# Optimization experiments

Measured on AMD Instinct MI355X. Metric: run time of the kernel, lower is better.

Reference implementation:

```python
import jax, jax.numpy as jnp
import numpy as np

IH = IW = 1024          # image size (iH, iW)
NMS_CAND = 1000         # dup_attrs['nms_candidates']
NMS_THR = 0.65          # dup_attrs['nms_thr']
MAX_SEGS = 100          # max_segs


def _mask_to_box(masks):
    # masks: [N, H, W] bool -> xyxy float boxes [N, 4] in pixel coords
    N, H, W = masks.shape
    rows = masks.any(axis=2)            # [N, H]
    cols = masks.any(axis=1)            # [N, W]
    x1 = jnp.argmax(cols, axis=1)
    x2 = W - jnp.argmax(cols[:, ::-1], axis=1)
    y1 = jnp.argmax(rows, axis=1)
    y2 = H - jnp.argmax(rows[:, ::-1], axis=1)
    return jnp.stack([x1, y1, x2, y2], axis=-1).astype(jnp.float32)


def _box_iou(b):
    # b: [K, 4] xyxy -> pairwise IoU [K, K]
    x1, y1, x2, y2 = b[:, 0], b[:, 1], b[:, 2], b[:, 3]
    area = (x2 - x1) * (y2 - y1)
    ix1 = jnp.maximum(x1[:, None], x1[None, :])
    iy1 = jnp.maximum(y1[:, None], y1[None, :])
    ix2 = jnp.minimum(x2[:, None], x2[None, :])
    iy2 = jnp.minimum(y2[:, None], y2[None, :])
    inter = jnp.clip(ix2 - ix1, 0.0) * jnp.clip(iy2 - iy1, 0.0)
    union = area[:, None] + area[None, :] - inter
    return inter / jnp.maximum(union, 1e-9)


def _greedy_nms_keep(iou, thr):
    # boxes assumed pre-sorted by descending score; returns keep mask [K]
    k = iou.shape[0]
    idx = jnp.arange(k)

    def body(i, keep):
        sup = keep[i] & (iou[i] > thr) & (idx > i)
        return keep & ~sup

    return jax.lax.fori_loop(0, k, body, jnp.ones((k,), dtype=bool))


def setup_inputs() -> dict:
    key = jax.random.key(0)
    k1, k2 = jax.random.split(key)
    cls_logits = jax.random.normal(k1, (300, 81), dtype=jnp.float32)
    seg_logits = jax.random.normal(k2, (300, 200, 200), dtype=jnp.float32)
    return {"cls_logits": cls_logits, "seg_logits": seg_logits}


def reference(cls_logits, seg_logits):
    N, fH, fW = seg_logits.shape
    C = cls_logits.shape[1] - 1  # last class is background/no-object

    # mask thresholding + emptiness flag (filtering replaced by score masking)
    pred_masks = seg_logits > 0                              # [N, fH, fW]
    non_empty = pred_masks.reshape(N, -1).sum(axis=1) > 0    # [N]

    # mask -> box for NMS
    boxes = _mask_to_box(pred_masks)                         # [N, 4]

    # sigmoid scoring over (feat, class); empty masks get score -1 (never picked)
    scores = jax.nn.sigmoid(cls_logits[:, :-1])              # [N, C]
    scores = jnp.where(non_empty[:, None], scores, -1.0).reshape(-1)  # [N*C]
    feat_ids = jnp.repeat(jnp.arange(N), C)                  # [N*C]
    labels = jnp.tile(jnp.arange(C), N)                      # [N*C]

    # top nms_candidates (scores sorted descending)
    k = min(NMS_CAND, N * C)
    cand_scores, cand_ids = jax.lax.top_k(scores, k)
    cand_feats = feat_ids[cand_ids]
    cand_labels = labels[cand_ids]
    cand_boxes = boxes[cand_feats]

    # batched (class-aware) NMS: offset boxes per label
    offset = cand_labels.astype(jnp.float32)[:, None] * (float(max(fH, fW)) + 1.0)
    iou = _box_iou(cand_boxes + offset)
    keep = _greedy_nms_keep(iou, NMS_THR) & (cand_scores >= 0.0)

    # keep top max_segs among survivors
    kept_scores = jnp.where(keep, cand_scores, -jnp.inf)
    sel_scores, sel = jax.lax.top_k(kept_scores, MAX_SEGS)
    sel_feats = cand_feats[sel]
    sel_labels = cand_labels[sel]

    # upsample selected mask logits to image size and threshold
    sel_logits = seg_logits[sel_feats]                       # [M, fH, fW]
    maps = jax.image.resize(sel_logits, (MAX_SEGS, IH, IW), method='bilinear')
    out_masks = maps > 0                                     # [M, iH, iW] bool
    batch_ids = jnp.zeros((MAX_SEGS,), dtype=jnp.int32)

    return sel_labels, out_masks, sel_scores, batch_ids
```

## Files before the change

kernel.cpp:

```cpp
#include <hip/hip_runtime.h>
#include <cstdint>
#include <cstddef>

typedef unsigned int u32;
typedef unsigned long long u64;
typedef float vf4 __attribute__((ext_vector_type(4)));

#define NF 300
#define NCLS 80
#define NCLS1 81
#define FH 200
#define FW 200
#define PIX 40000
#define NC 24000
#define KCAND 1000
#define CAP 4096
#define NBINS 65536
#define MAXSEG 100
#define OUT_MASK_OFF 100
#define OUT_SCORE_OFF 104857700
#define OUT_BATCH_OFF 104857800
#define NEG_BIG -3.3895313892515355e38f
#define RYC 8

#define WS_HIST      0u
#define WS_KEYS      262144u
#define WS_COLLECT   454144u
#define WS_CNT       486912u
#define WS_BOXES     486928u
#define WS_CLAB      496928u
#define WS_CFEAT     500928u
#define WS_CSCORE    504928u
#define WS_CBOX      508928u
#define WS_ROWBITS   524928u
#define WS_SELFEAT   656128u
#define WS_WTAB      656528u

__device__ __forceinline__ u32 ord32_r3(float f) {
  u32 b = __float_as_uint(f);
  return (b & 0x80000000u) ? ~b : (b | 0x80000000u);
}
__device__ __forceinline__ float unord32_r3(u32 o) {
  u32 b = (o & 0x80000000u) ? (o & 0x7FFFFFFFu) : ~o;
  return __uint_as_float(b);
}

__global__ void r3_init_wtab(u32* __restrict__ hist, u32* __restrict__ cnts,
                             float4* __restrict__ wtab) {
  int i = blockIdx.x * 256 + threadIdx.x;
  hist[i] = 0u;
  if (i < 4) cnts[i] = 0u;
  if (i < 1024) {
    float s = __fsub_rn(__fmul_rn((float)i + 0.5f, 0.1953125f), 0.5f);
    int j0 = (int)floorf(s);
    int j1 = j0 + 1;
    float w0 = fmaxf(0.f, __fsub_rn(1.f, fabsf(__fsub_rn(s, (float)j0))));
    float w1 = fmaxf(0.f, __fsub_rn(1.f, fabsf(__fsub_rn(s, (float)j1))));
    bool in0 = (j0 >= 0) && (j0 < FH);
    bool in1 = (j1 >= 0) && (j1 < FH);
    float tot = __fadd_rn(in0 ? w0 : 0.f, in1 ? w1 : 0.f);
    float w0n = in0 ? (w0 / tot) : 0.f;
    float w1n = in1 ? (w1 / tot) : 0.f;
    wtab[i] = make_float4(w0n, w1n, (float)max(j0, 0), (float)min(j1, FH - 1));
  }
}

__global__ void r3_boxes_scores(const float* __restrict__ seg, const float* __restrict__ cls,
                                float4* __restrict__ boxes, u64* __restrict__ keys,
                                u32* __restrict__ hist) {
  __shared__ int sminx[256], sminy[256], smaxx[256], smaxy[256];
  int n = blockIdx.x, t = threadIdx.x;
  const float4* img = (const float4*)(seg + (size_t)n * PIX);
  int minx = FW, miny = FH, maxx = -1, maxy = -1;
  for (int q = t; q < PIX / 4; q += 256) {
    float4 v = img[q];
    int p = q * 4;
    int y = p / FW;
    int x = p - y * FW;
    if (v.x > 0.f) { minx = min(minx, x);     maxx = max(maxx, x);     miny = min(miny, y); maxy = max(maxy, y); }
    if (v.y > 0.f) { minx = min(minx, x + 1); maxx = max(maxx, x + 1); miny = min(miny, y); maxy = max(maxy, y); }
    if (v.z > 0.f) { minx = min(minx, x + 2); maxx = max(maxx, x + 2); miny = min(miny, y); maxy = max(maxy, y); }
    if (v.w > 0.f) { minx = min(minx, x + 3); maxx = max(maxx, x + 3); miny = min(miny, y); maxy = max(maxy, y); }
  }
  sminx[t] = minx; sminy[t] = miny; smaxx[t] = maxx; smaxy[t] = maxy;
  __syncthreads();
  for (int s = 128; s > 0; s >>= 1) {
    if (t < s) {
      sminx[t] = min(sminx[t], sminx[t + s]);
      sminy[t] = min(sminy[t], sminy[t + s]);
      smaxx[t] = max(smaxx[t], smaxx[t + s]);
      smaxy[t] = max(smaxy[t], smaxy[t + s]);
    }
    __syncthreads();
  }
  bool ne = smaxx[0] >= 0;
  if (t == 0) {
    float4 b;
    if (ne) b = make_float4((float)sminx[0], (float)sminy[0], (float)(smaxx[0] + 1), (float)(smaxy[0] + 1));
    else    b = make_float4(0.f, 0.f, (float)FW, (float)FH);
    boxes[n] = b;
  }
  if (t < NCLS) {
    float sc;
    if (ne) {
      float lg = cls[n * NCLS1 + t];
      sc = 1.0f / (1.0f + expf(-lg));
    } else {
      sc = -1.0f;
    }
    u32 o = ord32_r3(sc);
    u32 i = (u32)(n * NCLS + t);
    keys[i] = ((u64)o << 32) | (u64)(0xFFFFFFFFu - i);
    atomicAdd(&hist[o >> 16], 1u);
  }
}

__global__ void r3_thresh(const u32* __restrict__ hist, u32* __restrict__ cnts) {
  __shared__ u32 s[1024];
  int t = threadIdx.x;
  u32 sum = 0;
  const u32* hp = hist + t * 64;
  for (int b = 0; b < 64; b++) sum += hp[b];
  s[t] = sum;
  __syncthreads();
  for (int off = 1; off < 1024; off <<= 1) {
    u32 v = s[t];
    u32 o = (t + off < 1024) ? s[t + off] : 0u;
    __syncthreads();
    s[t] = v + o;
    __syncthreads();
  }
  u32 sufnext = (t < 1023) ? s[t + 1] : 0u;
  if (s[t] >= (u32)KCAND && sufnext < (u32)KCAND) {
    u32 run = sufnext;
    u32 B = (u32)(t * 64);
    for (int b = 63; b >= 0; b--) {
      run += hist[t * 64 + b];
      if (run >= (u32)KCAND) { B = (u32)(t * 64 + b); break; }
    }
    cnts[1] = B;
  }
}

__global__ void r3_collect(const u64* __restrict__ keys, const u32* __restrict__ cnts,
                           u64* __restrict__ collect, u32* __restrict__ counter) {
  int i = blockIdx.x * 256 + threadIdx.x;
  if (i >= NC) return;
  u64 k = keys[i];
  if ((u32)(k >> 48) >= cnts[1]) {
    u32 pos = atomicAdd(counter, 1u);
    if (pos < CAP) collect[pos] = k;
  }
}

__global__ void r3_rank(const u64* __restrict__ collect, const u32* __restrict__ cnts,
                        const float4* __restrict__ boxes,
                        int* __restrict__ clab, int* __restrict__ cfeat,
                        float* __restrict__ cscore, float4* __restrict__ cbox) {
  __shared__ u64 sk[CAP];
  int M = min((int)cnts[0], CAP);
  int t = threadIdx.x;
  for (int j = t; j < M; j += 64) sk[j] = collect[j];
  __syncthreads();
  for (int j = blockIdx.x * 64 + t; j < M; j += 64 * 16) {
    u64 mykey = sk[j];
    int r = 0;
    for (int k = 0; k < M; k++) r += (sk[k] > mykey) ? 1 : 0;
    if (r < KCAND) {
      u32 idx = 0xFFFFFFFFu - (u32)(mykey & 0xFFFFFFFFull);
      int n = (int)idx / NCLS, c = (int)idx - n * NCLS;
      clab[r] = c;
      cfeat[r] = n;
      cscore[r] = unord32_r3((u32)(mykey >> 32));
      float4 b = boxes[n];
      float off = (float)c * 201.0f;
      cbox[r] = make_float4(b.x + off, b.y + off, b.z + off, b.w + off);
    }
  }
}

__global__ void r3_iou(const float4* __restrict__ cbox, u64* __restrict__ rowbits) {
  int i = blockIdx.x;
  int lane = threadIdx.x;
  float4 bi = make_float4(0.f, 0.f, 0.f, 0.f);
  float ai = 0.f;
  if (i < KCAND) { bi = cbox[i]; ai = (bi.z - bi.x) * (bi.w - bi.y); }
  for (int ch = 0; ch < 16; ch++) {
    int j = ch * 64 + lane;
    bool pred = false;
    if (i < KCAND && j < KCAND && j > i) {
      float4 bj = cbox[j];
      float aj = (bj.z - bj.x) * (bj.w - bj.y);
      float ix1 = fmaxf(bi.x, bj.x), iy1 = fmaxf(bi.y, bj.y);
      float ix2 = fminf(bi.z, bj.z), iy2 = fminf(bi.w, bj.w);
      float inter = fmaxf(ix2 - ix1, 0.f) * fmaxf(iy2 - iy1, 0.f);
      float uni = ai + aj - inter;
      float iou = inter / fmaxf(uni, 1e-9f);
      pred = iou > 0.65f;
    }
    u64 m = __ballot(pred);
    if (lane == 0) rowbits[(size_t)i * 16 + ch] = m;
  }
}

__global__ void r3_nms_sel(const u64* __restrict__ rowbits, const float* __restrict__ cscore,
                           const int* __restrict__ clab, const int* __restrict__ cfeat,
                           float* __restrict__ out, int* __restrict__ selfeat) {
  __shared__ u64 sup[16];
  __shared__ u64 keep[16];
  __shared__ u64 sk[KCAND];
  int t = threadIdx.x;
  if (t < 16) sup[t] = 0ull;
  __syncthreads();
  for (int c = 0; c < 16; c++) {
    if (t < 64) {
      int L = t;
      u64 r = rowbits[(size_t)(c * 64 + L) * 16 + c];
      u64 s = sup[c];
      u64 k = 0ull;
      #pragma unroll 4
      for (int b = 0; b < 64; b++) {
        u64 rb = __shfl(r, b, 64);
        if (!((s >> b) & 1ull)) { s |= rb; k |= (1ull << b); }
      }
      if (L == 0) { sup[c] = s; keep[c] = k; }
      if (L > c && L < 16) {
        u64 acc = sup[L];
        for (int b = 0; b < 64; b++)
          if ((k >> b) & 1ull) acc |= rowbits[(size_t)(c * 64 + b) * 16 + L];
        sup[L] = acc;
      }
    }
    __syncthreads();
  }
  for (int j = t; j < KCAND; j += 1024) {
    bool kp = ((keep[j >> 6] >> (j & 63)) & 1ull) != 0ull;
    float sc = cscore[j];
    u32 hi = (kp && sc >= 0.f) ? ord32_r3(sc) : 0u;
    sk[j] = ((u64)hi << 32) | (u64)(0xFFFFFFFFu - (u32)j);
  }
  __syncthreads();
  if (t < KCAND) {
    u64 my = sk[t];
    int r = 0;
    for (int k = 0; k < KCAND; k++) r += (sk[k] > my) ? 1 : 0;
    if (r < MAXSEG) {
      u32 hi = (u32)(my >> 32);
      float oscore = (hi == 0u) ? NEG_BIG : unord32_r3(hi);
      oscore = fmaxf(oscore, NEG_BIG);
      out[r] = (float)clab[t];
      out[OUT_SCORE_OFF + r] = oscore;
      out[OUT_BATCH_OFF + r] = 0.0f;
      selfeat[r] = cfeat[t];
    }
  }
}

__global__ void __launch_bounds__(256) r3_resize(const float* __restrict__ seg,
                                                 const int* __restrict__ selfeat,
                                                 const float4* __restrict__ wtab,
                                                 float* __restrict__ outm) {
  __shared__ float4 swx[1024];
  __shared__ float srow[4][FW];
  int t = threadIdx.x;
  int yb = blockIdx.x * RYC, slot = blockIdx.y;
  int feat = selfeat[slot];
  const float* img = seg + (size_t)feat * PIX;
  #pragma unroll
  for (int k = 0; k < 4; k++) swx[t + 256 * k] = wtab[t + 256 * k];
  int ylo = (int)wtab[yb].z;
  int yhi = (int)wtab[yb + RYC - 1].w;
  int nr = yhi - ylo + 1;
  for (int e = t; e < nr * FW; e += 256) {
    int rr = e / FW, cc = e - rr * FW;
    srow[rr][cc] = img[(ylo + rr) * FW + cc];
  }
  __syncthreads();
  int xb = t * 4;
  float4 wxa = swx[xb], wxb = swx[xb + 1], wxc = swx[xb + 2], wxd = swx[xb + 3];
  int xa0 = (int)wxa.z, xa1 = (int)wxa.w;
  int xb0 = (int)wxb.z, xb1 = (int)wxb.w;
  int xc0 = (int)wxc.z, xc1 = (int)wxc.w;
  int xd0 = (int)wxd.z, xd1 = (int)wxd.w;
  float* obase = outm + (size_t)slot * 1048576 + (size_t)yb * 1024 + xb;
  #pragma unroll
  for (int r = 0; r < RYC; r++) {
    int y = yb + r;
    float4 wy = wtab[y];
    const float* r0 = srow[(int)wy.z - ylo];
    const float* r1 = srow[(int)wy.w - ylo];
    float wy0 = wy.x, wy1 = wy.y;
    float ta0 = __fmaf_rn(wy1, r1[xa0], __fmul_rn(wy0, r0[xa0]));
    float ta1 = __fmaf_rn(wy1, r1[xa1], __fmul_rn(wy0, r0[xa1]));
    float va  = __fmaf_rn(wxa.y, ta1, __fmul_rn(wxa.x, ta0));
    float tb0 = __fmaf_rn(wy1, r1[xb0], __fmul_rn(wy0, r0[xb0]));
    float tb1 = __fmaf_rn(wy1, r1[xb1], __fmul_rn(wy0, r0[xb1]));
    float vb  = __fmaf_rn(wxb.y, tb1, __fmul_rn(wxb.x, tb0));
    float tc0 = __fmaf_rn(wy1, r1[xc0], __fmul_rn(wy0, r0[xc0]));
    float tc1 = __fmaf_rn(wy1, r1[xc1], __fmul_rn(wy0, r0[xc1]));
    float vc  = __fmaf_rn(wxc.y, tc1, __fmul_rn(wxc.x, tc0));
    float td0 = __fmaf_rn(wy1, r1[xd0], __fmul_rn(wy0, r0[xd0]));
    float td1 = __fmaf_rn(wy1, r1[xd1], __fmul_rn(wy0, r0[xd1]));
    float vd  = __fmaf_rn(wxd.y, td1, __fmul_rn(wxd.x, td0));
    vf4 res;
    res.x = (va > 0.0f) ? 1.0f : 0.0f;
    res.y = (vb > 0.0f) ? 1.0f : 0.0f;
    res.z = (vc > 0.0f) ? 1.0f : 0.0f;
    res.w = (vd > 0.0f) ? 1.0f : 0.0f;
    __builtin_nontemporal_store(res, (vf4*)(obase + (size_t)r * 1024));
  }
}

extern "C" void kernel_launch(void* const* d_in, const int* in_sizes, int n_in,
                              void* d_out, int out_size, void* d_ws, size_t ws_size,
                              hipStream_t stream) {
  const float* cls = (const float*)d_in[0];
  const float* seg = (const float*)d_in[1];
  float* out = (float*)d_out;
  char* ws = (char*)d_ws;

  u32* hist      = (u32*)(ws + WS_HIST);
  u64* keys      = (u64*)(ws + WS_KEYS);
  u64* collect   = (u64*)(ws + WS_COLLECT);
  u32* cnts      = (u32*)(ws + WS_CNT);
  float4* boxes  = (float4*)(ws + WS_BOXES);
  int* clab      = (int*)(ws + WS_CLAB);
  int* cfeat     = (int*)(ws + WS_CFEAT);
  float* cscore  = (float*)(ws + WS_CSCORE);
  float4* cbox   = (float4*)(ws + WS_CBOX);
  u64* rowbits   = (u64*)(ws + WS_ROWBITS);
  int* selfeat   = (int*)(ws + WS_SELFEAT);
  float4* wtab   = (float4*)(ws + WS_WTAB);

  r3_init_wtab<<<dim3(NBINS / 256), dim3(256), 0, stream>>>(hist, cnts, wtab);
  r3_boxes_scores<<<dim3(NF), dim3(256), 0, stream>>>(seg, cls, boxes, keys, hist);
  r3_thresh<<<dim3(1), dim3(1024), 0, stream>>>(hist, cnts);
  r3_collect<<<dim3((NC + 255) / 256), dim3(256), 0, stream>>>(keys, cnts, collect, &cnts[0]);
  r3_rank<<<dim3(16), dim3(64), 0, stream>>>(collect, cnts, boxes, clab, cfeat, cscore, cbox);
  r3_iou<<<dim3(1024), dim3(64), 0, stream>>>(cbox, rowbits);
  r3_nms_sel<<<dim3(1), dim3(1024), 0, stream>>>(rowbits, cscore, clab, cfeat, out, selfeat);
  r3_resize<<<dim3(1024 / RYC, MAXSEG), dim3(256), 0, stream>>>(seg, selfeat, wtab, out + OUT_MASK_OFF);
}
```

Measured before the change: 656.5 us.

## Fuse top-k selection into one block and compute resize weights inline

```diff
diff --git a/kernel.cpp b/kernel.cpp
--- a/kernel.cpp
+++ b/kernel.cpp
@@ -15,18 +15,15 @@
 #define NC 24000
 #define KCAND 1000
 #define CAP 4096
-#define NBINS 65536
+#define TBINS 4096
 #define MAXSEG 100
 #define OUT_MASK_OFF 100
 #define OUT_SCORE_OFF 104857700
 #define OUT_BATCH_OFF 104857800
 #define NEG_BIG -3.3895313892515355e38f
-#define RYC 8
-
-#define WS_HIST      0u
+#define RYC 16
+
 #define WS_KEYS      262144u
-#define WS_COLLECT   454144u
-#define WS_CNT       486912u
 #define WS_BOXES     486928u
 #define WS_CLAB      496928u
 #define WS_CFEAT     500928u
@@ -34,7 +31,6 @@
 #define WS_CBOX      508928u
 #define WS_ROWBITS   524928u
 #define WS_SELFEAT   656128u
-#define WS_WTAB      656528u
 
 __device__ __forceinline__ u32 ord32_r3(float f) {
   u32 b = __float_as_uint(f);
@@ -45,29 +41,22 @@
   return __uint_as_float(b);
 }
 
-__global__ void r3_init_wtab(u32* __restrict__ hist, u32* __restrict__ cnts,
-                             float4* __restrict__ wtab) {
-  int i = blockIdx.x * 256 + threadIdx.x;
-  hist[i] = 0u;
-  if (i < 4) cnts[i] = 0u;
-  if (i < 1024) {
-    float s = __fsub_rn(__fmul_rn((float)i + 0.5f, 0.1953125f), 0.5f);
-    int j0 = (int)floorf(s);
-    int j1 = j0 + 1;
-    float w0 = fmaxf(0.f, __fsub_rn(1.f, fabsf(__fsub_rn(s, (float)j0))));
-    float w1 = fmaxf(0.f, __fsub_rn(1.f, fabsf(__fsub_rn(s, (float)j1))));
-    bool in0 = (j0 >= 0) && (j0 < FH);
-    bool in1 = (j1 >= 0) && (j1 < FH);
-    float tot = __fadd_rn(in0 ? w0 : 0.f, in1 ? w1 : 0.f);
-    float w0n = in0 ? (w0 / tot) : 0.f;
-    float w1n = in1 ? (w1 / tot) : 0.f;
-    wtab[i] = make_float4(w0n, w1n, (float)max(j0, 0), (float)min(j1, FH - 1));
-  }
-}
-
-__global__ void r3_boxes_scores(const float* __restrict__ seg, const float* __restrict__ cls,
-                                float4* __restrict__ boxes, u64* __restrict__ keys,
-                                u32* __restrict__ hist) {
+__device__ __forceinline__ float4 wcalc_r4(int i) {
+  float s = __fsub_rn(__fmul_rn((float)i + 0.5f, 0.1953125f), 0.5f);
+  int j0 = (int)floorf(s);
+  int j1 = j0 + 1;
+  float w0 = fmaxf(0.f, __fsub_rn(1.f, fabsf(__fsub_rn(s, (float)j0))));
+  float w1 = fmaxf(0.f, __fsub_rn(1.f, fabsf(__fsub_rn(s, (float)j1))));
+  bool in0 = (j0 >= 0) && (j0 < FH);
+  bool in1 = (j1 >= 0) && (j1 < FH);
+  float tot = __fadd_rn(in0 ? w0 : 0.f, in1 ? w1 : 0.f);
+  float w0n = in0 ? (w0 / tot) : 0.f;
+  float w1n = in1 ? (w1 / tot) : 0.f;
+  return make_float4(w0n, w1n, (float)max(j0, 0), (float)min(j1, FH - 1));
+}
+
+__global__ void rb_boxes(const float* __restrict__ seg, const float* __restrict__ cls,
+                         float4* __restrict__ boxes, u64* __restrict__ keys) {
   __shared__ int sminx[256], sminy[256], smaxx[256], smaxy[256];
   int n = blockIdx.x, t = threadIdx.x;
   const float4* img = (const float4*)(seg + (size_t)n * PIX);
@@ -111,67 +100,66 @@
     u32 o = ord32_r3(sc);
     u32 i = (u32)(n * NCLS + t);
     keys[i] = ((u64)o << 32) | (u64)(0xFFFFFFFFu - i);
-    atomicAdd(&hist[o >> 16], 1u);
-  }
-}
-
-__global__ void r3_thresh(const u32* __restrict__ hist, u32* __restrict__ cnts) {
-  __shared__ u32 s[1024];
-  int t = threadIdx.x;
-  u32 sum = 0;
-  const u32* hp = hist + t * 64;
-  for (int b = 0; b < 64; b++) sum += hp[b];
-  s[t] = sum;
-  __syncthreads();
-  for (int off = 1; off < 1024; off <<= 1) {
-    u32 v = s[t];
-    u32 o = (t + off < 1024) ? s[t + off] : 0u;
-    __syncthreads();
-    s[t] = v + o;
-    __syncthreads();
-  }
-  u32 sufnext = (t < 1023) ? s[t + 1] : 0u;
-  if (s[t] >= (u32)KCAND && sufnext < (u32)KCAND) {
-    u32 run = sufnext;
-    u32 B = (u32)(t * 64);
-    for (int b = 63; b >= 0; b--) {
-      run += hist[t * 64 + b];
-      if (run >= (u32)KCAND) { B = (u32)(t * 64 + b); break; }
-    }
-    cnts[1] = B;
-  }
-}
-
-__global__ void r3_collect(const u64* __restrict__ keys, const u32* __restrict__ cnts,
-                           u64* __restrict__ collect, u32* __restrict__ counter) {
-  int i = blockIdx.x * 256 + threadIdx.x;
-  if (i >= NC) return;
-  u64 k = keys[i];
-  if ((u32)(k >> 48) >= cnts[1]) {
-    u32 pos = atomicAdd(counter, 1u);
-    if (pos < CAP) collect[pos] = k;
-  }
-}
-
-__global__ void r3_rank(const u64* __restrict__ collect, const u32* __restrict__ cnts,
-                        const float4* __restrict__ boxes,
+  }
+}
+
+__global__ void rt_topk(const u64* __restrict__ keys, const float4* __restrict__ boxes,
                         int* __restrict__ clab, int* __restrict__ cfeat,
                         float* __restrict__ cscore, float4* __restrict__ cbox) {
+  __shared__ u32 hist[TBINS];
   __shared__ u64 sk[CAP];
-  int M = min((int)cnts[0], CAP);
+  __shared__ u32 ssum[1024];
+  __shared__ u32 sB, scnt;
   int t = threadIdx.x;
-  for (int j = t; j < M; j += 64) sk[j] = collect[j];
-  __syncthreads();
-  for (int j = blockIdx.x * 64 + t; j < M; j += 64 * 16) {
-    u64 mykey = sk[j];
+  for (int b = t; b < TBINS; b += 1024) hist[b] = 0u;
+  if (t == 0) scnt = 0u;
+  __syncthreads();
+  for (int i = t; i < NC; i += 1024) {
+    u32 bin = (u32)(keys[i] >> 52);
+    atomicAdd(&hist[bin], 1u);
+  }
+  __syncthreads();
+  u32 sum = hist[4 * t] + hist[4 * t + 1] + hist[4 * t + 2] + hist[4 * t + 3];
+  ssum[t] = sum;
+  __syncthreads();
+  for (int off = 1; off < 1024; off <<= 1) {
+    u32 v = ssum[t];
+    u32 o = (t + off < 1024) ? ssum[t + off] : 0u;
+    __syncthreads();
+    ssum[t] = v + o;
+    __syncthreads();
+  }
+  u32 sufnext = (t < 1023) ? ssum[t + 1] : 0u;
+  if (ssum[t] >= (u32)KCAND && sufnext < (u32)KCAND) {
+    u32 run = sufnext;
+    u32 B = (u32)(4 * t);
+    for (int b = 3; b >= 0; b--) {
+      run += hist[4 * t + b];
+      if (run >= (u32)KCAND) { B = (u32)(4 * t + b); break; }
+    }
+    sB = B;
+  }
+  __syncthreads();
+  u32 B = sB;
+  for (int i = t; i < NC; i += 1024) {
+    u64 k = keys[i];
+    if ((u32)(k >> 52) >= B) {
+      u32 pos = atomicAdd(&scnt, 1u);
+      if (pos < CAP) sk[pos] = k;
+    }
+  }
+  __syncthreads();
+  int M = min((int)scnt, CAP);
+  for (int j = t; j < M; j += 1024) {
+    u64 my = sk[j];
     int r = 0;
-    for (int k = 0; k < M; k++) r += (sk[k] > mykey) ? 1 : 0;
+    for (int k = 0; k < M; k++) r += (sk[k] > my) ? 1 : 0;
     if (r < KCAND) {
-      u32 idx = 0xFFFFFFFFu - (u32)(mykey & 0xFFFFFFFFull);
+      u32 idx = 0xFFFFFFFFu - (u32)(my & 0xFFFFFFFFull);
       int n = (int)idx / NCLS, c = (int)idx - n * NCLS;
       clab[r] = c;
       cfeat[r] = n;
-      cscore[r] = unord32_r3((u32)(mykey >> 32));
+      cscore[r] = unord32_r3((u32)(my >> 32));
       float4 b = boxes[n];
       float off = (float)c * 201.0f;
       cbox[r] = make_float4(b.x + off, b.y + off, b.z + off, b.w + off);
@@ -226,8 +214,11 @@
       if (L == 0) { sup[c] = s; keep[c] = k; }
       if (L > c && L < 16) {
         u64 acc = sup[L];
-        for (int b = 0; b < 64; b++)
-          if ((k >> b) & 1ull) acc |= rowbits[(size_t)(c * 64 + b) * 16 + L];
+        #pragma unroll
+        for (int b = 0; b < 64; b++) {
+          u64 v = rowbits[(size_t)(c * 64 + b) * 16 + L];
+          if ((k >> b) & 1ull) acc |= v;
+        }
         sup[L] = acc;
       }
     }
@@ -256,20 +247,18 @@
   }
 }
 
-__global__ void __launch_bounds__(256) r3_resize(const float* __restrict__ seg,
+__global__ void __launch_bounds__(256) r4_resize(const float* __restrict__ seg,
                                                  const int* __restrict__ selfeat,
-                                                 const float4* __restrict__ wtab,
                                                  float* __restrict__ outm) {
-  __shared__ float4 swx[1024];
-  __shared__ float srow[4][FW];
+  __shared__ float srow[6][FW];
   int t = threadIdx.x;
   int yb = blockIdx.x * RYC, slot = blockIdx.y;
   int feat = selfeat[slot];
   const float* img = seg + (size_t)feat * PIX;
-  #pragma unroll
-  for (int k = 0; k < 4; k++) swx[t + 256 * k] = wtab[t + 256 * k];
-  int ylo = (int)wtab[yb].z;
-  int yhi = (int)wtab[yb + RYC - 1].w;
+  float4 wxa = wcalc_r4(t * 4), wxb = wcalc_r4(t * 4 + 1),
+         wxc = wcalc_r4(t * 4 + 2), wxd = wcalc_r4(t * 4 + 3);
+  int ylo = (int)wcalc_r4(yb).z;
+  int yhi = (int)wcalc_r4(yb + RYC - 1).w;
   int nr = yhi - ylo + 1;
   for (int e = t; e < nr * FW; e += 256) {
     int rr = e / FW, cc = e - rr * FW;
@@ -277,7 +266,6 @@
   }
   __syncthreads();
   int xb = t * 4;
-  float4 wxa = swx[xb], wxb = swx[xb + 1], wxc = swx[xb + 2], wxd = swx[xb + 3];
   int xa0 = (int)wxa.z, xa1 = (int)wxa.w;
   int xb0 = (int)wxb.z, xb1 = (int)wxb.w;
   int xc0 = (int)wxc.z, xc1 = (int)wxc.w;
@@ -285,8 +273,7 @@
   float* obase = outm + (size_t)slot * 1048576 + (size_t)yb * 1024 + xb;
   #pragma unroll
   for (int r = 0; r < RYC; r++) {
-    int y = yb + r;
-    float4 wy = wtab[y];
+    float4 wy = wcalc_r4(yb + r);
     const float* r0 = srow[(int)wy.z - ylo];
     const float* r1 = srow[(int)wy.w - ylo];
     float wy0 = wy.x, wy1 = wy.y;
@@ -307,7 +294,7 @@
     res.y = (vb > 0.0f) ? 1.0f : 0.0f;
     res.z = (vc > 0.0f) ? 1.0f : 0.0f;
     res.w = (vd > 0.0f) ? 1.0f : 0.0f;
-    __builtin_nontemporal_store(res, (vf4*)(obase + (size_t)r * 1024));
+    *(vf4*)(obase + (size_t)r * 1024) = res;
   }
 }
 
@@ -319,10 +306,7 @@
   float* out = (float*)d_out;
   char* ws = (char*)d_ws;
 
-  u32* hist      = (u32*)(ws + WS_HIST);
   u64* keys      = (u64*)(ws + WS_KEYS);
-  u64* collect   = (u64*)(ws + WS_COLLECT);
-  u32* cnts      = (u32*)(ws + WS_CNT);
   float4* boxes  = (float4*)(ws + WS_BOXES);
   int* clab      = (int*)(ws + WS_CLAB);
   int* cfeat     = (int*)(ws + WS_CFEAT);
@@ -330,14 +314,10 @@
   float4* cbox   = (float4*)(ws + WS_CBOX);
   u64* rowbits   = (u64*)(ws + WS_ROWBITS);
   int* selfeat   = (int*)(ws + WS_SELFEAT);
-  float4* wtab   = (float4*)(ws + WS_WTAB);
-
-  r3_init_wtab<<<dim3(NBINS / 256), dim3(256), 0, stream>>>(hist, cnts, wtab);
-  r3_boxes_scores<<<dim3(NF), dim3(256), 0, stream>>>(seg, cls, boxes, keys, hist);
-  r3_thresh<<<dim3(1), dim3(1024), 0, stream>>>(hist, cnts);
-  r3_collect<<<dim3((NC + 255) / 256), dim3(256), 0, stream>>>(keys, cnts, collect, &cnts[0]);
-  r3_rank<<<dim3(16), dim3(64), 0, stream>>>(collect, cnts, boxes, clab, cfeat, cscore, cbox);
+
+  rb_boxes<<<dim3(NF), dim3(256), 0, stream>>>(seg, cls, boxes, keys);
+  rt_topk<<<dim3(1), dim3(1024), 0, stream>>>(keys, boxes, clab, cfeat, cscore, cbox);
   r3_iou<<<dim3(1024), dim3(64), 0, stream>>>(cbox, rowbits);
   r3_nms_sel<<<dim3(1), dim3(1024), 0, stream>>>(rowbits, cscore, clab, cfeat, out, selfeat);
-  r3_resize<<<dim3(1024 / RYC, MAXSEG), dim3(256), 0, stream>>>(seg, selfeat, wtab, out + OUT_MASK_OFF);
-}
+  r4_resize<<<dim3(1024 / RYC, MAXSEG), dim3(256), 0, stream>>>(seg, selfeat, out + OUT_MASK_OFF);
+}
```

New measurement: 646.1 us. Within noise of the previous version (-1.6%).
